# Kernel tuning notes

Measured on AMD Instinct MI355X. Metric: run time of the kernel, lower is better.

Reference implementation:

```python
import jax, jax.numpy as jnp
import numpy as np

B, C, H, W = 1, 256, 96, 96
C8 = C // 8
N = H * W


def setup_inputs() -> dict:
    key = jax.random.key(0)
    ks = jax.random.split(key, 12)
    inp = {
        "x": jax.random.normal(ks[0], (B, C, H, W), jnp.float32),
        "x_encoder": jax.random.normal(ks[1], (B, C, H, W), jnp.float32),
        # 1x1 conv params (weight stored as [out, in] matrices)
        "q_w": jax.random.normal(ks[2], (C8, C), jnp.float32) * 0.05,
        "q_b": jax.random.normal(ks[3], (C8,), jnp.float32) * 0.05,
        "k_w": jax.random.normal(ks[4], (C8, C), jnp.float32) * 0.05,
        "k_b": jax.random.normal(ks[5], (C8,), jnp.float32) * 0.05,
        "v_w": jax.random.normal(ks[6], (C, C), jnp.float32) * 0.05,
        "v_b": jax.random.normal(ks[7], (C,), jnp.float32) * 0.05,
        # positional bias parameters
        "h_pos": jax.random.normal(ks[8], (1, C8, H, 1), jnp.float32),
        "w_pos": jax.random.normal(ks[9], (1, C8, 1, W), jnp.float32),
        # gamma is zero-init in the module; use a random scalar for a non-trivial test
        "gamma": jax.random.normal(ks[10], (1,), jnp.float32),
    }
    return inp


def reference(x, x_encoder, q_w, q_b, k_w, k_b, v_w, v_b, h_pos, w_pos, gamma):
    b, c, h, w = x.shape
    n = h * w
    c8 = q_w.shape[0]
    # 1x1 convs == per-pixel linear maps
    query = (jnp.einsum('bchw,oc->bohw', x, q_w) + q_b[None, :, None, None])
    query = query.reshape(b, c8, n).transpose(0, 2, 1)            # [B, N, C8]
    key = (jnp.einsum('bchw,oc->bohw', x_encoder, k_w) + k_b[None, :, None, None])
    key = key.reshape(b, c8, n)                                   # [B, C8, N]
    # positional bias: broadcast-add then flatten, same as (height+width).view
    pos = (h_pos + w_pos).reshape(1, c8, n)                       # [1, C8, N]
    # energy = Q K^T + Q pos  ==  Q (K + pos)
    energy = jnp.einsum('bnc,bcm->bnm', query, key + pos)         # [B, N, N]
    attention = jax.nn.softmax(energy, axis=-1)
    value = (jnp.einsum('bchw,oc->bohw', x_encoder, v_w) + v_b[None, :, None, None])
    value = value.reshape(b, c, n)                                # [B, C, N]
    out = jnp.einsum('bcm,bnm->bcn', value, attention)            # [B, C, N]
    out = out.reshape(b, c, w, h)  # matches torch .view(B, C, W, H)
    return gamma * out + x
```

## Files before the change

### kernel.cpp

```cpp
#include <hip/hip_runtime.h>
#include <hip/hip_bf16.h>

#define NN 9216
#define CC 256
#define LOG2E 1.4426950408889634f

typedef __attribute__((ext_vector_type(8))) short short8;
typedef __attribute__((ext_vector_type(16))) float floatx16;
typedef __attribute__((ext_vector_type(4))) float floatx4;
typedef __attribute__((ext_vector_type(4))) unsigned short ushortx4;

#if __has_builtin(__builtin_amdgcn_exp2f)
#define fexp2 __builtin_amdgcn_exp2f
#else
#define fexp2 exp2f
#endif

__device__ __forceinline__ unsigned short f2bf(float f) {
    unsigned u = __float_as_uint(f);
    u = u + 0x7fffu + ((u >> 16) & 1u);
    return (unsigned short)(u >> 16);
}
__device__ __forceinline__ float bf2f(unsigned short s) {
    return __uint_as_float(((unsigned)s) << 16);
}
__device__ __forceinline__ unsigned pack2bf(float a, float b) {
    union { __hip_bfloat162 h; unsigned u; } cv;
    cv.h = __float22bfloat162_rn(make_float2(a, b));
    return cv.u;
}
__device__ __forceinline__ floatx16 mfma_bf16(short8 a, short8 b, floatx16 c) {
    return __builtin_amdgcn_mfma_f32_32x32x16_bf16(a, b, c, 0, 0, 0);
}

__global__ __launch_bounds__(256) void prep(
    const float* __restrict__ x, const float* __restrict__ xe,
    short* __restrict__ XBhi, short* __restrict__ XBlo,
    short* __restrict__ EBhi, short* __restrict__ EBlo)
{
    int t = threadIdx.x;
    const float* in = blockIdx.y ? xe : x;
    short* Dhi = blockIdx.y ? EBhi : XBhi;
    short* Dlo = blockIdx.y ? EBlo : XBlo;
    int tl = t & 31, sub = t >> 5;
    int nt = blockIdx.x >> 2, q4 = blockIdx.x & 3;
    int sub2 = q4 * 8 + sub;
    int kb_ = sub2 >> 1, hl = sub2 & 1;
    int n = nt * 32 + tl;
    int c0 = kb_ * 16 + hl * 8;
    union { unsigned short us[8]; short8 v8; } hi, lo;
#pragma unroll
    for (int j = 0; j < 8; ++j) {
        float val = in[(size_t)(c0 + j) * NN + n];
        unsigned short hb = f2bf(val);
        hi.us[j] = hb;
        lo.us[j] = f2bf(val - bf2f(hb));
    }
    size_t off = (((size_t)nt * 16 + kb_) * 64 + hl * 32 + tl) * 8;
    *(short8*)(Dhi + off) = hi.v8;
    *(short8*)(Dlo + off) = lo.v8;
}

__global__ __launch_bounds__(256) void wprep(
    const float* __restrict__ qw, const float* __restrict__ kw,
    const float* __restrict__ vw,
    short* __restrict__ WAhi, short* __restrict__ WAlo)
{
    int g = blockIdx.x * 256 + threadIdx.x;
    int lane = g & 63, kb_ = (g >> 6) & 15, ot = g >> 10;
    int o = lane & 31, half = lane >> 5;
    int c0 = kb_ * 16 + half * 8;
    const float* wsrc;
    int orow;
    float scale = 1.f;
    if (ot == 0) { wsrc = qw; orow = o; scale = LOG2E; }
    else if (ot == 1) { wsrc = kw; orow = o; }
    else { wsrc = vw; orow = (ot - 2) * 32 + o; }
    union { unsigned short us[8]; short8 v8; } hi, lo;
#pragma unroll
    for (int j = 0; j < 8; ++j) {
        float val = wsrc[(size_t)orow * 256 + c0 + j] * scale;
        unsigned short hb = f2bf(val);
        hi.us[j] = hb;
        lo.us[j] = f2bf(val - bf2f(hb));
    }
    size_t off = (((size_t)ot * 16 + kb_) * 64 + lane) * 8;
    *(short8*)(WAhi + off) = hi.v8;
    *(short8*)(WAlo + off) = lo.v8;
}

__global__ __launch_bounds__(256) void gemm_all(
    const short* __restrict__ XBhi, const short* __restrict__ XBlo,
    const short* __restrict__ EBhi, const short* __restrict__ EBlo,
    const short* __restrict__ WAhi, const short* __restrict__ WAlo,
    const float* __restrict__ qb, const float* __restrict__ kb,
    const float* __restrict__ hpos, const float* __restrict__ wpos,
    const float* __restrict__ vb,
    short* __restrict__ Qhi, short* __restrict__ Qlo,
    short* __restrict__ KP2, short* __restrict__ VF)
{
    __shared__ float lds[4][1024];
    int t = threadIdx.x;
    int wv = t >> 6, lane = t & 63, ln = lane & 31, h = lane >> 5;
    int nt = blockIdx.x * 2 + (wv & 1);
    int tile = blockIdx.y * 2 + (wv >> 1);

    const short* Bhi = (tile == 0 ? XBhi : EBhi) + (size_t)nt * 8192 + lane * 8;
    const short* Blo = (tile == 0 ? XBlo : EBlo) + (size_t)nt * 8192 + lane * 8;
    const short* Ahi = WAhi + (size_t)tile * 8192 + lane * 8;
    const short* Alo = WAlo + (size_t)tile * 8192 + lane * 8;

    floatx16 D;
#pragma unroll
    for (int r = 0; r < 16; ++r) D[r] = 0.f;
#pragma unroll
    for (int k = 0; k < 16; ++k) {
        short8 bh = *(const short8*)(Bhi + k * 512);
        short8 bl = *(const short8*)(Blo + k * 512);
        short8 ah = *(const short8*)(Ahi + k * 512);
        short8 al = *(const short8*)(Alo + k * 512);
        D = mfma_bf16(ah, bh, D);
        D = mfma_bf16(ah, bl, D);
        D = mfma_bf16(al, bh, D);
    }

    float* L = lds[wv];
#pragma unroll
    for (int r = 0; r < 16; ++r) {
        int row = (r & 3) + 8 * (r >> 2) + 4 * h;
        L[row * 32 + ((ln + row) & 31)] = D[r];
    }
    __syncthreads();

    if (tile == 0) {
        int n = nt * 32 + ln;
#pragma unroll
        for (int it = 0; it < 2; ++it) {
            int j0 = it * 16 + h * 8;
            union { unsigned short us[8]; short8 v8; } qh_, ql_;
#pragma unroll
            for (int jj = 0; jj < 8; ++jj) {
                int row = j0 + jj;
                float d = L[row * 32 + ((ln + row) & 31)] + qb[row] * LOG2E;
                unsigned short hb = f2bf(d);
                qh_.us[jj] = hb;
                ql_.us[jj] = f2bf(d - bf2f(hb));
            }
            *(short8*)(Qhi + (size_t)n * 32 + j0) = qh_.v8;
            *(short8*)(Qlo + (size_t)n * 32 + j0) = ql_.v8;
        }
    } else if (tile == 1) {
        int n = nt * 32 + ln;
        int hh = ((n >> 5) * 683) >> 11;
        int ww = n - hh * 96;
#pragma unroll
        for (int it = 0; it < 2; ++it) {
            int jb0 = it * 16 + h * 8;
            union { unsigned short us[8]; short8 v8; } o;
#pragma unroll
            for (int jj = 0; jj < 8; ++jj) {
                int row = jb0 + jj;
                float d = L[row * 32 + ((ln + row) & 31)]
                        + kb[row] + hpos[row * 96 + hh] + wpos[row * 96 + ww];
                o.us[jj] = f2bf(d);
            }
            *(short8*)(KP2 + (size_t)nt * 1024 + it * 512 + h * 256 + ln * 8) = o.v8;
        }
    } else {
        int cc = tile - 2;
        float bias = vb[cc * 32 + ln];
#pragma unroll
        for (int it = 0; it < 2; ++it) {
            union { unsigned short us[8]; short8 v8; } o;
#pragma unroll
            for (int ee = 0; ee < 8; ++ee) {
                int ml = it * 16 + h * 8 + ee;
                float d = L[ln * 32 + ((ml + ln) & 31)];
                o.us[ee] = f2bf(d + bias);
            }
            *(short8*)(VF + ((size_t)(nt * 2 + it) * 8 + cc) * 512 + lane * 8) = o.v8;
        }
    }
}

#define SMPV(S, V0, V1, V2, V3, U0, U1, U2, U3, OA, OB, OC, OD, LACC) do {            \
    float ps = 0.f;                                                                   \
    _Pragma("unroll") for (int r = 0; r < 16; ++r) { S[r] = fexp2(S[r]); ps += S[r]; } \
    ps += __shfl_xor(ps, 32); LACC += ps;                                             \
    unsigned w0 = pack2bf(S[0], S[1]),  w1 = pack2bf(S[2], S[3]);                     \
    unsigned w2 = pack2bf(S[4], S[5]),  w3 = pack2bf(S[6], S[7]);                     \
    unsigned w4 = pack2bf(S[8], S[9]),  w5 = pack2bf(S[10], S[11]);                   \
    unsigned w6 = pack2bf(S[12], S[13]), w7 = pack2bf(S[14], S[15]);                  \
    {   unsigned p0 = h ? w0 : w2, p1 = h ? w1 : w3;                                  \
        unsigned e0 = (unsigned)__shfl_xor((int)p0, 32);                              \
        unsigned e1 = (unsigned)__shfl_xor((int)p1, 32);                              \
        union { unsigned u[4]; short8 v; } pf;                                        \
        pf.u[0] = h ? e0 : w0; pf.u[1] = h ? e1 : w1;                                 \
        pf.u[2] = h ? w2 : e0; pf.u[3] = h ? w3 : e1;                                 \
        OA = mfma_bf16(V0, pf.v, OA); OB = mfma_bf16(V1, pf.v, OB);                   \
        OC = mfma_bf16(V2, pf.v, OC); OD = mfma_bf16(V3, pf.v, OD); }                 \
    {   unsigned p0 = h ? w4 : w6, p1 = h ? w5 : w7;                                  \
        unsigned e0 = (unsigned)__shfl_xor((int)p0, 32);                              \
        unsigned e1 = (unsigned)__shfl_xor((int)p1, 32);                              \
        union { unsigned u[4]; short8 v; } pf;                                        \
        pf.u[0] = h ? e0 : w4; pf.u[1] = h ? e1 : w5;                                 \
        pf.u[2] = h ? w6 : e0; pf.u[3] = h ? w7 : e1;                                 \
        OA = mfma_bf16(U0, pf.v, OA); OB = mfma_bf16(U1, pf.v, OB);                   \
        OC = mfma_bf16(U2, pf.v, OC); OD = mfma_bf16(U3, pf.v, OD); }                 \
} while (0)

#define OGW2(CF, T, OG) { _Pragma("unroll") for (int r = 0; r < 16; ++r) {            \
    int row = ch * 128 + (CF) * 32 + (r & 3) + 8 * (r >> 2) + 4 * h;                  \
    Opart[obase + (size_t)row * NN + n0 + (T) * 32 + ln] = f2bf(OG[r]); } }

__global__ __launch_bounds__(128, 2) void flash(
    const short* __restrict__ Qhi, const short* __restrict__ Qlo,
    const short* __restrict__ KP2, const short* __restrict__ VF,
    unsigned short* __restrict__ Opart, float* __restrict__ Lpart)
{
    int t = threadIdx.x;
    int wv = t >> 6;
    int lane = t & 63;
    int ln = lane & 31;
    int h = lane >> 5;
    int bx = blockIdx.x;
    int ntp = bx >> 3, mq = (bx >> 1) & 3, ch = bx & 1;
    int n0 = ntp * 128 + wv * 64;
    int mstart = mq * 2304;

    int qoffA = (n0 + ln) * 32 + h * 8;
    int qoffB = (n0 + 32 + ln) * 32 + h * 8;
    short8 qAh0 = *(const short8*)(Qhi + qoffA);
    short8 qAl0 = *(const short8*)(Qlo + qoffA);
    short8 qAh1 = *(const short8*)(Qhi + qoffA + 16);
    short8 qAl1 = *(const short8*)(Qlo + qoffA + 16);
    short8 qBh0 = *(const short8*)(Qhi + qoffB);
    short8 qBl0 = *(const short8*)(Qlo + qoffB);
    short8 qBh1 = *(const short8*)(Qhi + qoffB + 16);
    short8 qBl1 = *(const short8*)(Qlo + qoffB + 16);

    const short* Vb  = VF + (size_t)(mstart >> 4) * 4096 + ch * 2048 + lane * 8;
    const short* KPb = KP2 + (size_t)mstart * 32 + lane * 8;

    floatx16 O00, O10, O20, O30, O01, O11, O21, O31;
#pragma unroll
    for (int r = 0; r < 16; ++r) {
        O00[r] = 0.f; O10[r] = 0.f; O20[r] = 0.f; O30[r] = 0.f;
        O01[r] = 0.f; O11[r] = 0.f; O21[r] = 0.f; O31[r] = 0.f;
    }
    float l0 = 0.f, l1 = 0.f;

    short8 ah0 = *(const short8*)(KPb);
    short8 ah1 = *(const short8*)(KPb + 512);

    for (int sp = 0; sp < 72; ++sp) {
        const short* Vp = Vb + (size_t)sp * 8192;
        short8 vf00 = *(const short8*)(Vp);
        short8 vf10 = *(const short8*)(Vp + 512);
        short8 vf20 = *(const short8*)(Vp + 1024);
        short8 vf30 = *(const short8*)(Vp + 1536);
        short8 vf01 = *(const short8*)(Vp + 4096);
        short8 vf11 = *(const short8*)(Vp + 4608);
        short8 vf21 = *(const short8*)(Vp + 5120);
        short8 vf31 = *(const short8*)(Vp + 5632);

        int nm = (sp < 71) ? sp + 1 : 0;
        short8 an0 = *(const short8*)(KPb + (size_t)nm * 1024);
        short8 an1 = *(const short8*)(KPb + (size_t)nm * 1024 + 512);

        floatx16 SA = {0.f,0.f,0.f,0.f,0.f,0.f,0.f,0.f,0.f,0.f,0.f,0.f,0.f,0.f,0.f,0.f};
        SA = mfma_bf16(ah0, qAh0, SA);
        SA = mfma_bf16(ah0, qAl0, SA);
        SA = mfma_bf16(ah1, qAh1, SA);
        SA = mfma_bf16(ah1, qAl1, SA);
        SMPV(SA, vf00, vf10, vf20, vf30, vf01, vf11, vf21, vf31,
             O00, O10, O20, O30, l0);

        floatx16 SB = {0.f,0.f,0.f,0.f,0.f,0.f,0.f,0.f,0.f,0.f,0.f,0.f,0.f,0.f,0.f,0.f};
        SB = mfma_bf16(ah0, qBh0, SB);
        SB = mfma_bf16(ah0, qBl0, SB);
        SB = mfma_bf16(ah1, qBh1, SB);
        SB = mfma_bf16(ah1, qBl1, SB);
        SMPV(SB, vf00, vf10, vf20, vf30, vf01, vf11, vf21, vf31,
             O01, O11, O21, O31, l1);

        ah0 = an0; ah1 = an1;
    }

    if (ch == 0 && lane < 32) {
        Lpart[mq * NN + n0 + ln] = l0;
        Lpart[mq * NN + n0 + 32 + ln] = l1;
    }
    size_t obase = (size_t)mq * ((size_t)CC * NN);
    OGW2(0, 0, O00) OGW2(1, 0, O10) OGW2(2, 0, O20) OGW2(3, 0, O30)
    OGW2(0, 1, O01) OGW2(1, 1, O11) OGW2(2, 1, O21) OGW2(3, 1, O31)
}

__global__ __launch_bounds__(256) void stats(
    const float* __restrict__ Lpart, const float* __restrict__ gamma,
    float* __restrict__ W)
{
    int n = blockIdx.x * 256 + threadIdx.x;
    float L = Lpart[n] + Lpart[NN + n] + Lpart[2 * NN + n] + Lpart[3 * NN + n];
    W[n] = gamma[0] / L;
}

__global__ __launch_bounds__(256) void combine(
    const unsigned short* __restrict__ Opart, const float* __restrict__ W,
    const float* __restrict__ x, float* __restrict__ out)
{
    int i = blockIdx.x * 256 + threadIdx.x;
    int flat = i * 4;
    int n = flat % NN;
    floatx4 acc = *(const floatx4*)&x[flat];
    floatx4 w = *(const floatx4*)&W[n];
    float s0 = 0.f, s1 = 0.f, s2 = 0.f, s3 = 0.f;
#pragma unroll
    for (int q = 0; q < 4; ++q) {
        ushortx4 o = *(const ushortx4*)(Opart + (size_t)q * ((size_t)CC * NN) + flat);
        s0 += bf2f(o[0]); s1 += bf2f(o[1]); s2 += bf2f(o[2]); s3 += bf2f(o[3]);
    }
    acc[0] += s0 * w[0]; acc[1] += s1 * w[1]; acc[2] += s2 * w[2]; acc[3] += s3 * w[3];
    *(floatx4*)&out[flat] = acc;
}

extern "C" void kernel_launch(void* const* d_in, const int* in_sizes, int n_in,
                              void* d_out, int out_size, void* d_ws, size_t ws_size,
                              hipStream_t stream) {
    const float* x  = (const float*)d_in[0];
    const float* xe = (const float*)d_in[1];
    const float* qw = (const float*)d_in[2];
    const float* qb = (const float*)d_in[3];
    const float* kw = (const float*)d_in[4];
    const float* kb = (const float*)d_in[5];
    const float* vw = (const float*)d_in[6];
    const float* vb = (const float*)d_in[7];
    const float* hp = (const float*)d_in[8];
    const float* wp = (const float*)d_in[9];
    const float* gm = (const float*)d_in[10];

    char* ws = (char*)d_ws;
    short* Qhi  = (short*)(ws + 0);
    short* Qlo  = (short*)(ws + 589824);
    short* KP2  = (short*)(ws + 1179648);
    short* WAhi = (short*)(ws + 1769472);
    short* WAlo = (short*)(ws + 1933312);
    short* VF   = (short*)(ws + 2097152);
    unsigned short* Opart = (unsigned short*)(ws + 6815744);
    short* XBhi = (short*)(ws + 6815744);
    short* XBlo = (short*)(ws + 11534336);
    short* EBhi = (short*)(ws + 16252928);
    short* EBlo = (short*)(ws + 20971520);
    float* Lpart = (float*)(ws + 25837568);
    float* W     = (float*)(ws + 25985024);

    prep<<<dim3(1152, 2), dim3(256), 0, stream>>>(x, xe, XBhi, XBlo, EBhi, EBlo);
    wprep<<<dim3(40), dim3(256), 0, stream>>>(qw, kw, vw, WAhi, WAlo);
    gemm_all<<<dim3(144, 5), dim3(256), 0, stream>>>(
        XBhi, XBlo, EBhi, EBlo, WAhi, WAlo, qb, kb, hp, wp, vb, Qhi, Qlo, KP2, VF);
    flash<<<dim3(576), dim3(128), 0, stream>>>(Qhi, Qlo, KP2, VF, Opart, Lpart);
    stats<<<dim3(36), dim3(256), 0, stream>>>(Lpart, gm, W);
    combine<<<dim3(2304), dim3(256), 0, stream>>>(Opart, W, x, (float*)d_out);
}
```

Baseline: 135.2 us.

## Stage K and V tiles through double-buffered LDS with async global-to-LDS loads

The flash kernel now loads each K/V tile into a double-buffered shared-memory area using global_load_lds direct copies, prefetching the next tile while computing the current one. The work split also changes: each block's two waves now share the same 64 query rows and each wave takes one half of the channels, where before each wave handled its own 64 rows. This halves redundant K loads per block and lets the copy overlap compute. In exchange it adds a block barrier every iteration, about 36 KB of LDS per block, and drops the launch_bounds occupancy hint.

```diff
diff --git a/kernel.cpp b/kernel.cpp
--- a/kernel.cpp
+++ b/kernel.cpp
@@ -31,6 +31,11 @@
 }
 __device__ __forceinline__ floatx16 mfma_bf16(short8 a, short8 b, floatx16 c) {
     return __builtin_amdgcn_mfma_f32_32x32x16_bf16(a, b, c, 0, 0, 0);
+}
+__device__ __forceinline__ void gload16(void* l, const void* g) {
+    __builtin_amdgcn_global_load_lds(
+        (const __attribute__((address_space(1))) unsigned int*)g,
+        (__attribute__((address_space(3))) unsigned int*)l, 16, 0, 0);
 }
 
 __global__ __launch_bounds__(256) void prep(
@@ -183,53 +188,74 @@
     }
 }
 
-#define SMPV(S, V0, V1, V2, V3, U0, U1, U2, U3, OA, OB, OC, OD, LACC) do {            \
-    float ps = 0.f;                                                                   \
+#define STAGE(B, SP) do {                                                          \
+    const char* vs_ = Vg + (size_t)(SP) * 16384 + wv * 8192 + lane * 16;           \
+    char* vd_ = (char*)(&sbuf[(B)][0]) + wv * 8192;                                \
+    gload16(vd_,        vs_);                                                      \
+    gload16(vd_ + 1024, vs_ + 1024);                                               \
+    gload16(vd_ + 2048, vs_ + 2048);                                               \
+    gload16(vd_ + 3072, vs_ + 3072);                                               \
+    gload16(vd_ + 4096, vs_ + 4096);                                               \
+    gload16(vd_ + 5120, vs_ + 5120);                                               \
+    gload16(vd_ + 6144, vs_ + 6144);                                               \
+    gload16(vd_ + 7168, vs_ + 7168);                                               \
+    gload16((char*)(&sbuf[(B)][8192]) + wv * 1024,                                 \
+            Kg + (size_t)(SP) * 2048 + wv * 1024 + lane * 16);                     \
+} while (0)
+
+#define NTSTEP(QH0, QL0, QH1, QL1, OA, OB, OC, OD, LACC) do {                      \
+    floatx16 S = {0.f,0.f,0.f,0.f,0.f,0.f,0.f,0.f,0.f,0.f,0.f,0.f,0.f,0.f,0.f,0.f}; \
+    S = mfma_bf16(ah0, QH0, S);                                                    \
+    S = mfma_bf16(ah0, QL0, S);                                                    \
+    S = mfma_bf16(ah1, QH1, S);                                                    \
+    S = mfma_bf16(ah1, QL1, S);                                                    \
+    float ps = 0.f;                                                                \
     _Pragma("unroll") for (int r = 0; r < 16; ++r) { S[r] = fexp2(S[r]); ps += S[r]; } \
-    ps += __shfl_xor(ps, 32); LACC += ps;                                             \
-    unsigned w0 = pack2bf(S[0], S[1]),  w1 = pack2bf(S[2], S[3]);                     \
-    unsigned w2 = pack2bf(S[4], S[5]),  w3 = pack2bf(S[6], S[7]);                     \
-    unsigned w4 = pack2bf(S[8], S[9]),  w5 = pack2bf(S[10], S[11]);                   \
-    unsigned w6 = pack2bf(S[12], S[13]), w7 = pack2bf(S[14], S[15]);                  \
-    {   unsigned p0 = h ? w0 : w2, p1 = h ? w1 : w3;                                  \
-        unsigned e0 = (unsigned)__shfl_xor((int)p0, 32);                              \
-        unsigned e1 = (unsigned)__shfl_xor((int)p1, 32);                              \
-        union { unsigned u[4]; short8 v; } pf;                                        \
-        pf.u[0] = h ? e0 : w0; pf.u[1] = h ? e1 : w1;                                 \
-        pf.u[2] = h ? w2 : e0; pf.u[3] = h ? w3 : e1;                                 \
-        OA = mfma_bf16(V0, pf.v, OA); OB = mfma_bf16(V1, pf.v, OB);                   \
-        OC = mfma_bf16(V2, pf.v, OC); OD = mfma_bf16(V3, pf.v, OD); }                 \
-    {   unsigned p0 = h ? w4 : w6, p1 = h ? w5 : w7;                                  \
-        unsigned e0 = (unsigned)__shfl_xor((int)p0, 32);                              \
-        unsigned e1 = (unsigned)__shfl_xor((int)p1, 32);                              \
-        union { unsigned u[4]; short8 v; } pf;                                        \
-        pf.u[0] = h ? e0 : w4; pf.u[1] = h ? e1 : w5;                                 \
-        pf.u[2] = h ? w6 : e0; pf.u[3] = h ? w7 : e1;                                 \
-        OA = mfma_bf16(U0, pf.v, OA); OB = mfma_bf16(U1, pf.v, OB);                   \
-        OC = mfma_bf16(U2, pf.v, OC); OD = mfma_bf16(U3, pf.v, OD); }                 \
+    ps += __shfl_xor(ps, 32); LACC += ps;                                          \
+    unsigned w0 = pack2bf(S[0], S[1]),  w1 = pack2bf(S[2], S[3]);                  \
+    unsigned w2 = pack2bf(S[4], S[5]),  w3 = pack2bf(S[6], S[7]);                  \
+    unsigned w4 = pack2bf(S[8], S[9]),  w5 = pack2bf(S[10], S[11]);                \
+    unsigned w6 = pack2bf(S[12], S[13]), w7 = pack2bf(S[14], S[15]);               \
+    {   unsigned p0 = h ? w0 : w2, p1 = h ? w1 : w3;                               \
+        unsigned e0 = (unsigned)__shfl_xor((int)p0, 32);                           \
+        unsigned e1 = (unsigned)__shfl_xor((int)p1, 32);                           \
+        union { unsigned u[4]; short8 v; } pf;                                     \
+        pf.u[0] = h ? e0 : w0; pf.u[1] = h ? e1 : w1;                              \
+        pf.u[2] = h ? w2 : e0; pf.u[3] = h ? w3 : e1;                              \
+        OA = mfma_bf16(v00, pf.v, OA); OB = mfma_bf16(v01, pf.v, OB);              \
+        OC = mfma_bf16(v02, pf.v, OC); OD = mfma_bf16(v03, pf.v, OD); }            \
+    {   unsigned p0 = h ? w4 : w6, p1 = h ? w5 : w7;                               \
+        unsigned e0 = (unsigned)__shfl_xor((int)p0, 32);                           \
+        unsigned e1 = (unsigned)__shfl_xor((int)p1, 32);                           \
+        union { unsigned u[4]; short8 v; } pf;                                     \
+        pf.u[0] = h ? e0 : w4; pf.u[1] = h ? e1 : w5;                              \
+        pf.u[2] = h ? w6 : e0; pf.u[3] = h ? w7 : e1;                              \
+        OA = mfma_bf16(v10, pf.v, OA); OB = mfma_bf16(v11, pf.v, OB);              \
+        OC = mfma_bf16(v12, pf.v, OC); OD = mfma_bf16(v13, pf.v, OD); }            \
 } while (0)
 
-#define OGW2(CF, T, OG) { _Pragma("unroll") for (int r = 0; r < 16; ++r) {            \
-    int row = ch * 128 + (CF) * 32 + (r & 3) + 8 * (r >> 2) + 4 * h;                  \
-    Opart[obase + (size_t)row * NN + n0 + (T) * 32 + ln] = f2bf(OG[r]); } }
-
-__global__ __launch_bounds__(128, 2) void flash(
+#define OGW(CF, NT, OG) { _Pragma("unroll") for (int r = 0; r < 16; ++r) {         \
+    int row = wv * 128 + (CF) * 32 + (r & 3) + 8 * (r >> 2) + 4 * h;               \
+    Opart[obase + (size_t)row * NN + n0 + (NT) * 32 + ln] = f2bf(OG[r]); } }
+
+__global__ __launch_bounds__(128) void flash(
     const short* __restrict__ Qhi, const short* __restrict__ Qlo,
     const short* __restrict__ KP2, const short* __restrict__ VF,
     unsigned short* __restrict__ Opart, float* __restrict__ Lpart)
 {
+    __shared__ short sbuf[2][9216];
     int t = threadIdx.x;
     int wv = t >> 6;
     int lane = t & 63;
     int ln = lane & 31;
     int h = lane >> 5;
     int bx = blockIdx.x;
-    int ntp = bx >> 3, mq = (bx >> 1) & 3, ch = bx & 1;
-    int n0 = ntp * 128 + wv * 64;
+    int ntb = bx >> 2, mq = bx & 3;
+    int n0 = ntb * 64;
     int mstart = mq * 2304;
 
     int qoffA = (n0 + ln) * 32 + h * 8;
-    int qoffB = (n0 + 32 + ln) * 32 + h * 8;
+    int qoffB = qoffA + 32 * 32;
     short8 qAh0 = *(const short8*)(Qhi + qoffA);
     short8 qAl0 = *(const short8*)(Qlo + qoffA);
     short8 qAh1 = *(const short8*)(Qhi + qoffA + 16);
@@ -239,61 +265,51 @@
     short8 qBh1 = *(const short8*)(Qhi + qoffB + 16);
     short8 qBl1 = *(const short8*)(Qlo + qoffB + 16);
 
-    const short* Vb  = VF + (size_t)(mstart >> 4) * 4096 + ch * 2048 + lane * 8;
-    const short* KPb = KP2 + (size_t)mstart * 32 + lane * 8;
-
-    floatx16 O00, O10, O20, O30, O01, O11, O21, O31;
+    const char* Vg = (const char*)VF + (size_t)(mstart >> 4) * 8192;
+    const char* Kg = (const char*)KP2 + (size_t)(mstart >> 5) * 2048;
+
+    floatx16 OA0, OA1, OA2, OA3, OB0, OB1, OB2, OB3;
 #pragma unroll
     for (int r = 0; r < 16; ++r) {
-        O00[r] = 0.f; O10[r] = 0.f; O20[r] = 0.f; O30[r] = 0.f;
-        O01[r] = 0.f; O11[r] = 0.f; O21[r] = 0.f; O31[r] = 0.f;
-    }
-    float l0 = 0.f, l1 = 0.f;
-
-    short8 ah0 = *(const short8*)(KPb);
-    short8 ah1 = *(const short8*)(KPb + 512);
+        OA0[r] = 0.f; OA1[r] = 0.f; OA2[r] = 0.f; OA3[r] = 0.f;
+        OB0[r] = 0.f; OB1[r] = 0.f; OB2[r] = 0.f; OB3[r] = 0.f;
+    }
+    float lA = 0.f, lB = 0.f;
+
+    int cur = 0;
+    STAGE(0, 0);
+    __syncthreads();
 
     for (int sp = 0; sp < 72; ++sp) {
-        const short* Vp = Vb + (size_t)sp * 8192;
-        short8 vf00 = *(const short8*)(Vp);
-        short8 vf10 = *(const short8*)(Vp + 512);
-        short8 vf20 = *(const short8*)(Vp + 1024);
-        short8 vf30 = *(const short8*)(Vp + 1536);
-        short8 vf01 = *(const short8*)(Vp + 4096);
-        short8 vf11 = *(const short8*)(Vp + 4608);
-        short8 vf21 = *(const short8*)(Vp + 5120);
-        short8 vf31 = *(const short8*)(Vp + 5632);
-
-        int nm = (sp < 71) ? sp + 1 : 0;
-        short8 an0 = *(const short8*)(KPb + (size_t)nm * 1024);
-        short8 an1 = *(const short8*)(KPb + (size_t)nm * 1024 + 512);
-
-        floatx16 SA = {0.f,0.f,0.f,0.f,0.f,0.f,0.f,0.f,0.f,0.f,0.f,0.f,0.f,0.f,0.f,0.f};
-        SA = mfma_bf16(ah0, qAh0, SA);
-        SA = mfma_bf16(ah0, qAl0, SA);
-        SA = mfma_bf16(ah1, qAh1, SA);
-        SA = mfma_bf16(ah1, qAl1, SA);
-        SMPV(SA, vf00, vf10, vf20, vf30, vf01, vf11, vf21, vf31,
-             O00, O10, O20, O30, l0);
-
-        floatx16 SB = {0.f,0.f,0.f,0.f,0.f,0.f,0.f,0.f,0.f,0.f,0.f,0.f,0.f,0.f,0.f,0.f};
-        SB = mfma_bf16(ah0, qBh0, SB);
-        SB = mfma_bf16(ah0, qBl0, SB);
-        SB = mfma_bf16(ah1, qBh1, SB);
-        SB = mfma_bf16(ah1, qBl1, SB);
-        SMPV(SB, vf00, vf10, vf20, vf30, vf01, vf11, vf21, vf31,
-             O01, O11, O21, O31, l1);
-
-        ah0 = an0; ah1 = an1;
-    }
-
-    if (ch == 0 && lane < 32) {
-        Lpart[mq * NN + n0 + ln] = l0;
-        Lpart[mq * NN + n0 + 32 + ln] = l1;
+        if (sp < 71) STAGE(cur ^ 1, sp + 1);
+
+        const short* vbase = &sbuf[cur][0] + wv * 2048;
+        const short* kbase = &sbuf[cur][8192];
+        short8 ah0 = *(const short8*)(kbase + lane * 8);
+        short8 ah1 = *(const short8*)(kbase + 512 + lane * 8);
+        short8 v00 = *(const short8*)(vbase + lane * 8);
+        short8 v01 = *(const short8*)(vbase + 512 + lane * 8);
+        short8 v02 = *(const short8*)(vbase + 1024 + lane * 8);
+        short8 v03 = *(const short8*)(vbase + 1536 + lane * 8);
+        short8 v10 = *(const short8*)(vbase + 4096 + lane * 8);
+        short8 v11 = *(const short8*)(vbase + 4608 + lane * 8);
+        short8 v12 = *(const short8*)(vbase + 5120 + lane * 8);
+        short8 v13 = *(const short8*)(vbase + 5632 + lane * 8);
+
+        NTSTEP(qAh0, qAl0, qAh1, qAl1, OA0, OA1, OA2, OA3, lA);
+        NTSTEP(qBh0, qBl0, qBh1, qBl1, OB0, OB1, OB2, OB3, lB);
+
+        __syncthreads();
+        cur ^= 1;
+    }
+
+    if (wv == 0 && lane < 32) {
+        Lpart[mq * NN + n0 + ln] = lA;
+        Lpart[mq * NN + n0 + 32 + ln] = lB;
     }
     size_t obase = (size_t)mq * ((size_t)CC * NN);
-    OGW2(0, 0, O00) OGW2(1, 0, O10) OGW2(2, 0, O20) OGW2(3, 0, O30)
-    OGW2(0, 1, O01) OGW2(1, 1, O11) OGW2(2, 1, O21) OGW2(3, 1, O31)
+    OGW(0, 0, OA0) OGW(1, 0, OA1) OGW(2, 0, OA2) OGW(3, 0, OA3)
+    OGW(0, 1, OB0) OGW(1, 1, OB1) OGW(2, 1, OB2) OGW(3, 1, OB3)
 }
 
 __global__ __launch_bounds__(256) void stats(
```

Result: slower. 192.9 us (+42.6%).
